# Optimization experiments

Measured on AMD Instinct MI355X. Metric: run time of the kernel, lower is better.

The kernel has to match this reference:

```python
import jax, jax.numpy as jnp
import numpy as np

NEG_BIG = -1e9

def setup_inputs() -> dict:
    key = jax.random.key(0)
    kq, kk, kv, kwq, kwk, kwv, km = jax.random.split(key, 7)
    B, S, d = 16, 1024, 512
    Q = jax.random.normal(kq, (B, S, d), dtype=jnp.float32)
    K = jax.random.normal(kk, (B, S, d), dtype=jnp.float32)
    V = jax.random.normal(kv, (B, S, d), dtype=jnp.float32)
    # nn.Linear weights [d, d]; torch applies x @ W.T
    WQ = jax.random.normal(kwq, (d, d), dtype=jnp.float32) / np.sqrt(d)
    WK = jax.random.normal(kwk, (d, d), dtype=jnp.float32) / np.sqrt(d)
    WV = jax.random.normal(kwv, (d, d), dtype=jnp.float32) / np.sqrt(d)
    mask = jax.random.randint(km, (B, S), 0, 2, dtype=jnp.int32)
    return {"Q": Q, "K": K, "V": V, "WQ": WQ, "WK": WK, "WV": WV, "mask": mask}


def reference(Q, K, V, WQ, WK, WV, mask):
    d = Q.shape[-1]
    q = jnp.einsum('bsd,ed->bse', Q, WQ)
    k = jnp.einsum('bsd,ed->bse', K, WK)
    v = jnp.einsum('bsd,ed->bse', V, WV)
    scores = jnp.einsum('bqd,bkd->bqk', q, k) / jnp.sqrt(jnp.float32(d))
    attn = jax.nn.softmax(scores, axis=-1)
    # Faithful to original: mask applied AFTER softmax with -1e9 fill
    m = mask[:, None, :]  # [B,1,S] broadcast over query dim
    attn = jnp.where(m == 0, jnp.float32(NEG_BIG), attn)
    out = jnp.einsum('bqk,bkd->bqd', attn, v)
    return (out, attn)
```

## Files before the change

### kernel.cpp

```cpp
#include <hip/hip_runtime.h>
#include <hip/hip_bf16.h>

typedef float f32x4 __attribute__((ext_vector_type(4)));
typedef __bf16 bf16x8 __attribute__((ext_vector_type(8)));
typedef unsigned short u16x8 __attribute__((ext_vector_type(8)));
typedef unsigned short u16x4 __attribute__((ext_vector_type(4)));
typedef int i32x4 __attribute__((ext_vector_type(4)));

#define NEG_BIG_F (-1000000000.0f)
#define SCALE_F 0.044194173824159216f

__device__ __forceinline__ unsigned short f2bf(float f) {
  unsigned int u = __float_as_uint(f);
  u += 0x7FFFu + ((u >> 16) & 1u);
  return (unsigned short)(u >> 16);
}

__device__ __forceinline__ float bf2f(unsigned short h) {
  return __uint_as_float((unsigned int)h << 16);
}

__device__ __forceinline__ u16x8 cvt8(f32x4 a, f32x4 b) {
  u16x8 r;
  r[0] = f2bf(a[0]); r[1] = f2bf(a[1]); r[2] = f2bf(a[2]); r[3] = f2bf(a[3]);
  r[4] = f2bf(b[0]); r[5] = f2bf(b[1]); r[6] = f2bf(b[2]); r[7] = f2bf(b[3]);
  return r;
}

__device__ __forceinline__ void gload16(const void* g, char* l) {
  __builtin_amdgcn_global_load_lds(
      (const __attribute__((address_space(1))) unsigned int*)g,
      (__attribute__((address_space(3))) unsigned int*)l, 16, 0, 0);
}

__global__ __launch_bounds__(256) void cvtWX(
    const float* __restrict__ w0, const float* __restrict__ w1,
    const float* __restrict__ w2, const float* __restrict__ Q,
    const float* __restrict__ Kx, const float* __restrict__ V,
    unsigned short* __restrict__ wb, unsigned short* __restrict__ xb)
{
  const int z = blockIdx.z;
  if (z == 0) {
    if (blockIdx.x >= 384) return;
    const int i = (blockIdx.x * 256 + threadIdx.x) * 8;
    const float* src = i < 262144 ? w0 : (i < 524288 ? w1 : w2);
    const int j = i & 262143;
    f32x4 a = *(const f32x4*)(src + j);
    f32x4 b = *(const f32x4*)(src + j + 4);
    *(u16x8*)&wb[i] = cvt8(a, b);
  } else {
    const float* src = z == 1 ? Q : (z == 2 ? Kx : V);
    unsigned short* dst = xb + (size_t)(z - 1) * 8388608;
    const int i = (blockIdx.x * 256 + threadIdx.x) * 8;
    f32x4 a = *(const f32x4*)(src + i);
    f32x4 b = *(const f32x4*)(src + i + 4);
    *(u16x8*)&dst[i] = cvt8(a, b);
  }
}

__global__ __launch_bounds__(512, 2) void proj_all(
    const unsigned short* __restrict__ xb, const unsigned short* __restrict__ wb,
    unsigned short* __restrict__ qb, unsigned short* __restrict__ kb,
    unsigned short* __restrict__ vt)
{
  __shared__ __align__(16) unsigned short As[2][256][32];
  __shared__ __align__(16) unsigned short Bs[2][256][32];

  const int bid = blockIdx.x;
  const int tid = threadIdx.x;
  const int lane = tid & 63, wave = tid >> 6;
  const int wr = (wave >> 2) * 128, wc = (wave & 3) * 64;
  const int fr = lane & 15, fq = lane >> 4;

  const unsigned short* Abase;
  const unsigned short* Bbase;
  int m0, n0;
  if (bid < 256) {
    const int z = bid >> 7, rem = bid & 127;
    m0 = (rem & 63) * 256; n0 = (rem >> 6) * 256;
    Abase = xb + (size_t)z * 8388608 + (size_t)m0 * 512;
    Bbase = wb + (size_t)z * 262144 + (size_t)n0 * 512;
  } else {
    const int c0 = bid - 256;
    const int b = c0 >> 3;
    m0 = ((c0 >> 2) & 1) * 256;
    n0 = (c0 & 3) * 256;
    Abase = wb + 524288 + (size_t)m0 * 512;
    Bbase = xb + 16777216 + ((size_t)b * 1024 + n0) * 512;
  }

  f32x4 acc[8][4] = {};

  const unsigned short* gA[2]; char* lA[2];
  const unsigned short* gB[2]; char* lB[2];
  #pragma unroll
  for (int i = 0; i < 2; i++) {
    const int c = tid + 512 * i, row = c >> 2, slot = c & 3;
    const int sw = (slot ^ ((row >> 1) & 3)) * 8;
    gA[i] = Abase + (size_t)row * 512 + sw;
    gB[i] = Bbase + (size_t)row * 512 + sw;
    lA[i] = (char*)&As[0][0][0] + c * 16;
    lB[i] = (char*)&Bs[0][0][0] + c * 16;
  }

  #pragma unroll
  for (int i = 0; i < 2; i++) { gload16(gA[i], lA[i]); gload16(gB[i], lB[i]); }

  int cur = 0;
  for (int kt = 0; kt < 512; kt += 32) {
    const int nb = cur ^ 1;
    if (kt < 480) {
      #pragma unroll
      for (int i = 0; i < 2; i++) {
        gload16(gA[i] + kt + 32, lA[i] + nb * 16384);
        gload16(gB[i] + kt + 32, lB[i] + nb * 16384);
      }
      asm volatile("s_waitcnt vmcnt(4) lgkmcnt(0)" ::: "memory");
    } else {
      asm volatile("s_waitcnt vmcnt(0) lgkmcnt(0)" ::: "memory");
    }
    __builtin_amdgcn_sched_barrier(0);
    __builtin_amdgcn_s_barrier();

    bf16x8 bv[4];
    #pragma unroll
    for (int nf = 0; nf < 4; nf++) {
      const int br = wc + nf * 16 + fr;
      bv[nf] = *(const bf16x8*)&Bs[cur][br][(fq ^ ((br >> 1) & 3)) * 8];
    }
    #pragma unroll
    for (int mf = 0; mf < 8; mf++) {
      const int ar = wr + mf * 16 + fr;
      bf16x8 av = *(const bf16x8*)&As[cur][ar][(fq ^ ((ar >> 1) & 3)) * 8];
      #pragma unroll
      for (int nf = 0; nf < 4; nf++)
        acc[mf][nf] = __builtin_amdgcn_mfma_f32_16x16x32_bf16(av, bv[nf], acc[mf][nf], 0, 0, 0);
    }
    __builtin_amdgcn_s_barrier();
    cur = nb;
  }

  if (bid < 256) {
    unsigned short* Y = (bid >> 7) ? kb : qb;
    #pragma unroll
    for (int mf = 0; mf < 8; mf++)
      #pragma unroll
      for (int nf = 0; nf < 4; nf++)
        #pragma unroll
        for (int rr = 0; rr < 4; rr++) {
          const int m = m0 + wr + mf * 16 + fq * 4 + rr;
          const int n = n0 + wc + nf * 16 + fr;
          Y[(size_t)m * 512 + n] = f2bf(acc[mf][nf][rr]);
        }
  } else {
    const int b = (bid - 256) >> 3;
    #pragma unroll
    for (int mf = 0; mf < 8; mf++)
      #pragma unroll
      for (int nf = 0; nf < 4; nf++)
        #pragma unroll
        for (int rr = 0; rr < 4; rr++) {
          const int e = m0 + wr + mf * 16 + fq * 4 + rr;
          const int s = n0 + wc + nf * 16 + fr;
          vt[((size_t)b * 512 + e) * 1024 + s] = f2bf(acc[mf][nf][rr]);
        }
  }
}

__global__ __launch_bounds__(512, 2) void score_mv(
    const unsigned short* __restrict__ qb, const unsigned short* __restrict__ kb,
    const unsigned short* __restrict__ vt, const int* __restrict__ mask,
    unsigned short* __restrict__ P, float* __restrict__ partial,
    float* __restrict__ mvsum)
{
  __shared__ __align__(16) unsigned short As[2][256][32];
  __shared__ __align__(16) unsigned short Bs[2][256][32];

  const int bid = blockIdx.x;
  const int tid = threadIdx.x;

  if (bid >= 256) {
    const int row = (bid - 256) * 8 + (tid >> 6);
    const int b = row >> 9;
    const int lane = tid & 63;
    const unsigned short* vr = vt + (size_t)row * 1024 + lane * 16;
    const int* mr = mask + b * 1024 + lane * 16;
    u16x8 v0 = *(const u16x8*)(vr);
    u16x8 v1 = *(const u16x8*)(vr + 8);
    float s = 0.f;
    #pragma unroll
    for (int j = 0; j < 8; j++) {
      if (!mr[j])     s += bf2f(v0[j]);
      if (!mr[8 + j]) s += bf2f(v1[j]);
    }
    #pragma unroll
    for (int o = 32; o > 0; o >>= 1) s += __shfl_xor(s, o);
    if (lane == 0) mvsum[row] = s;
    return;
  }

  const int xcd = bid & 7, idx = bid >> 3;
  const int bz = xcd * 2 + (idx >> 4);
  const int tile = idx & 15;
  const int m0 = (tile & 3) * 256, n0 = ((tile >> 2) & 3) * 256;
  const int lane = tid & 63, wave = tid >> 6;
  const int wr = (wave >> 2) * 128, wc = (wave & 3) * 64;
  const int fr = lane & 15, fq = lane >> 4;

  f32x4 acc[8][4] = {};

  const unsigned short* gA[2]; char* lA[2];
  const unsigned short* gB[2]; char* lB[2];
  #pragma unroll
  for (int i = 0; i < 2; i++) {
    const int c = tid + 512 * i, row = c >> 2, slot = c & 3;
    const int sw = (slot ^ ((row >> 1) & 3)) * 8;
    gA[i] = qb + ((size_t)bz * 1024 + m0 + row) * 512 + sw;
    gB[i] = kb + ((size_t)bz * 1024 + n0 + row) * 512 + sw;
    lA[i] = (char*)&As[0][0][0] + c * 16;
    lB[i] = (char*)&Bs[0][0][0] + c * 16;
  }

  #pragma unroll
  for (int i = 0; i < 2; i++) { gload16(gA[i], lA[i]); gload16(gB[i], lB[i]); }

  int cur = 0;
  for (int kt = 0; kt < 512; kt += 32) {
    const int nb = cur ^ 1;
    if (kt < 480) {
      #pragma unroll
      for (int i = 0; i < 2; i++) {
        gload16(gA[i] + kt + 32, lA[i] + nb * 16384);
        gload16(gB[i] + kt + 32, lB[i] + nb * 16384);
      }
      asm volatile("s_waitcnt vmcnt(4) lgkmcnt(0)" ::: "memory");
    } else {
      asm volatile("s_waitcnt vmcnt(0) lgkmcnt(0)" ::: "memory");
    }
    __builtin_amdgcn_sched_barrier(0);
    __builtin_amdgcn_s_barrier();

    bf16x8 bv[4];
    #pragma unroll
    for (int nf = 0; nf < 4; nf++) {
      const int br = wc + nf * 16 + fr;
      bv[nf] = *(const bf16x8*)&Bs[cur][br][(fq ^ ((br >> 1) & 3)) * 8];
    }
    #pragma unroll
    for (int mf = 0; mf < 8; mf++) {
      const int ar = wr + mf * 16 + fr;
      bf16x8 av = *(const bf16x8*)&As[cur][ar][(fq ^ ((ar >> 1) & 3)) * 8];
      #pragma unroll
      for (int nf = 0; nf < 4; nf++)
        acc[mf][nf] = __builtin_amdgcn_mfma_f32_16x16x32_bf16(av, bv[nf], acc[mf][nf], 0, 0, 0);
    }
    __builtin_amdgcn_s_barrier();
    cur = nb;
  }

  int mcol[4];
  #pragma unroll
  for (int nf = 0; nf < 4; nf++)
    mcol[nf] = mask[bz * 1024 + n0 + wc + nf * 16 + fr];

  unsigned short* Pb = P + ((size_t)bz << 20);
  const int slot = ((tile >> 2) & 3) * 4 + (wave & 3);
  #pragma unroll
  for (int mf = 0; mf < 8; mf++) {
    #pragma unroll
    for (int rr = 0; rr < 4; rr++) {
      const int m = m0 + wr + mf * 16 + fq * 4 + rr;
      float e = 0.f;
      #pragma unroll
      for (int nf = 0; nf < 4; nf++) {
        const float ev = __expf(acc[mf][nf][rr] * SCALE_F);
        e += ev;
        Pb[(size_t)m * 1024 + n0 + wc + nf * 16 + fr] =
            mcol[nf] ? f2bf(ev) : (unsigned short)0;
      }
      e += __shfl_xor(e, 1); e += __shfl_xor(e, 2);
      e += __shfl_xor(e, 4); e += __shfl_xor(e, 8);
      if (fr == 0)
        partial[(size_t)slot * 16384 + bz * 1024 + m] = e;
    }
  }
}

__global__ __launch_bounds__(512) void pv_attn(
    const unsigned short* __restrict__ P, const unsigned short* __restrict__ vt,
    const float* __restrict__ partial, const float* __restrict__ mvsum,
    const int* __restrict__ mask,
    float* __restrict__ out, float* __restrict__ attn)
{
  __shared__ __align__(16) unsigned short As[2][64][32];
  __shared__ __align__(16) unsigned short Bs[2][512][32];
  __shared__ float inv_l[64];

  const int tid = threadIdx.x;
  const int lin = blockIdx.x;
  const int xcd = lin & 7, idx = lin >> 3;
  const int bz = xcd * 2 + (idx >> 4);
  const int m0 = (idx & 15) * 64;
  const int lane = tid & 63, wave = tid >> 6;
  const int n0 = wave * 64;
  const int fr = lane & 15, fq = lane >> 4;

  f32x4 acc[4][4] = {};

  if (tid < 64) {
    float s = 0.f;
    #pragma unroll
    for (int p = 0; p < 16; p++) s += partial[(size_t)p * 16384 + bz * 1024 + m0 + tid];
    inv_l[tid] = 1.0f / s;
  }

  const unsigned short* gA = nullptr; char* lA = nullptr;
  if (tid < 256) {
    const int row = tid >> 2, slot = tid & 3;
    gA = P + ((size_t)bz << 20) + (size_t)(m0 + row) * 1024 + (slot ^ ((row >> 1) & 3)) * 8;
    lA = (char*)&As[0][0][0] + tid * 16;
  }
  const unsigned short* gB[4]; char* lB[4];
  #pragma unroll
  for (int i = 0; i < 4; i++) {
    const int c = tid + 512 * i, row = c >> 2, slot = c & 3;
    gB[i] = vt + ((size_t)bz * 512 + row) * 1024 + (slot ^ ((row >> 1) & 3)) * 8;
    lB[i] = (char*)&Bs[0][0][0] + c * 16;
  }

  const int arow = tid >> 3, acol = (tid & 7) * 4;
  const int aslot8 = ((acol >> 3) ^ ((arow >> 1) & 3)) * 8 + (acol & 7);
  float* arp = attn + ((size_t)bz * 1024 + m0 + arow) * 1024 + acol;
  const int* mrp = mask + bz * 1024 + acol;

  if (tid < 256) gload16(gA, lA);
  #pragma unroll
  for (int i = 0; i < 4; i++) gload16(gB[i], lB[i]);
  __syncthreads();

  int cur = 0;
  for (int t = 0; t < 32; t++) {
    const int nb = cur ^ 1;
    const int kt = t * 32;
    if (t < 31) {
      if (tid < 256) gload16(gA + kt + 32, lA + nb * 4096);
      #pragma unroll
      for (int i = 0; i < 4; i++) gload16(gB[i] + kt + 32, lB[i] + nb * 32768);
      if (wave < 4) asm volatile("s_waitcnt vmcnt(5) lgkmcnt(0)" ::: "memory");
      else          asm volatile("s_waitcnt vmcnt(4) lgkmcnt(0)" ::: "memory");
    } else {
      asm volatile("s_waitcnt vmcnt(0) lgkmcnt(0)" ::: "memory");
    }
    __builtin_amdgcn_sched_barrier(0);
    __builtin_amdgcn_s_barrier();

    bf16x8 af[4], bv[4];
    #pragma unroll
    for (int mf = 0; mf < 4; mf++) {
      const int ar = mf * 16 + fr;
      af[mf] = *(const bf16x8*)&As[cur][ar][(fq ^ ((ar >> 1) & 3)) * 8];
    }
    #pragma unroll
    for (int nf = 0; nf < 4; nf++) {
      const int br = n0 + nf * 16 + fr;
      bv[nf] = *(const bf16x8*)&Bs[cur][br][(fq ^ ((br >> 1) & 3)) * 8];
    }
    #pragma unroll
    for (int mf = 0; mf < 4; mf++)
      #pragma unroll
      for (int nf = 0; nf < 4; nf++)
        acc[mf][nf] = __builtin_amdgcn_mfma_f32_16x16x32_bf16(af[mf], bv[nf], acc[mf][nf], 0, 0, 0);

    {
      const u16x4 pv4 = *(const u16x4*)&As[cur][arow][aslot8];
      const i32x4 mv = *(const i32x4*)(mrp + kt);
      const float iv = inv_l[arow];
      f32x4 o;
      o[0] = mv[0] ? bf2f(pv4[0]) * iv : NEG_BIG_F;
      o[1] = mv[1] ? bf2f(pv4[1]) * iv : NEG_BIG_F;
      o[2] = mv[2] ? bf2f(pv4[2]) * iv : NEG_BIG_F;
      o[3] = mv[3] ? bf2f(pv4[3]) * iv : NEG_BIG_F;
      *(f32x4*)(arp + kt) = o;
    }
    __builtin_amdgcn_s_barrier();
    cur = nb;
  }

  float mvv[4];
  #pragma unroll
  for (int nf = 0; nf < 4; nf++)
    mvv[nf] = mvsum[bz * 512 + n0 + nf * 16 + fr];
  #pragma unroll
  for (int mf = 0; mf < 4; mf++)
    #pragma unroll
    for (int rr = 0; rr < 4; rr++) {
      const int m = m0 + mf * 16 + fq * 4 + rr;
      const float iv = inv_l[mf * 16 + fq * 4 + rr];
      #pragma unroll
      for (int nf = 0; nf < 4; nf++)
        out[((size_t)bz * 1024 + m) * 512 + n0 + nf * 16 + fr] =
            iv * acc[mf][nf][rr] + NEG_BIG_F * mvv[nf];
    }
}

extern "C" void kernel_launch(void* const* d_in, const int* in_sizes, int n_in,
                              void* d_out, int out_size, void* d_ws, size_t ws_size,
                              hipStream_t stream)
{
  const float* Q  = (const float*)d_in[0];
  const float* Kx = (const float*)d_in[1];
  const float* V  = (const float*)d_in[2];
  const float* WQ = (const float*)d_in[3];
  const float* WK = (const float*)d_in[4];
  const float* WV = (const float*)d_in[5];
  const int* mask = (const int*)d_in[6];

  const int B = 16, S = 1024, D = 512;
  float* out_f  = (float*)d_out;
  float* attn_f = out_f + (size_t)B * S * D;
  unsigned short* Pbuf = (unsigned short*)d_out;
  unsigned short* xb = (unsigned short*)attn_f;

  unsigned short* qb = (unsigned short*)d_ws;
  unsigned short* kb = qb + (size_t)B * S * D;
  unsigned short* vt = kb + (size_t)B * S * D;
  unsigned short* wb = vt + (size_t)B * S * D;
  float* partial = (float*)(wb + 786432);
  float* mvsum = partial + 262144;

  cvtWX<<<dim3(4096, 1, 4), 256, 0, stream>>>(WQ, WK, WV, Q, Kx, V, wb, xb);
  proj_all<<<dim3(384), 512, 0, stream>>>(xb, wb, qb, kb, vt);
  score_mv<<<dim3(1280), 512, 0, stream>>>(qb, kb, vt, mask, Pbuf, partial, mvsum);
  pv_attn<<<dim3(256), 512, 0, stream>>>(Pbuf, vt, partial, mvsum, mask, out_f, attn_f);
}
```

Measured before the change: 138.1 us.

## Fuse V fp32-to-bf16 conversion into the V projection GEMM

The separate conversion pass no longer converts V to bf16. The V-projection blocks in proj_all now stream fp32 V straight into LDS and convert to bf16 in registers before the MFMA. The V tiles shrink to 128x256 and the grid grows to 512 blocks, so LDS use rises to 80KB with fp32 B tiles. This removes one read and one write of V in bf16, at the cost of more LDS traffic and in-loop conversion work, and possibly lower occupancy.

```diff
diff --git a/kernel.cpp b/kernel.cpp
--- a/kernel.cpp
+++ b/kernel.cpp
@@ -27,6 +27,10 @@
   return r;
 }
 
+__device__ __forceinline__ bf16x8 u2b(u16x8 u) {
+  union { u16x8 u; bf16x8 b; } c; c.u = u; return c.b;
+}
+
 __device__ __forceinline__ void gload16(const void* g, char* l) {
   __builtin_amdgcn_global_load_lds(
       (const __attribute__((address_space(1))) unsigned int*)g,
@@ -36,7 +40,7 @@
 __global__ __launch_bounds__(256) void cvtWX(
     const float* __restrict__ w0, const float* __restrict__ w1,
     const float* __restrict__ w2, const float* __restrict__ Q,
-    const float* __restrict__ Kx, const float* __restrict__ V,
+    const float* __restrict__ Kx,
     unsigned short* __restrict__ wb, unsigned short* __restrict__ xb)
 {
   const int z = blockIdx.z;
@@ -49,7 +53,7 @@
     f32x4 b = *(const f32x4*)(src + j + 4);
     *(u16x8*)&wb[i] = cvt8(a, b);
   } else {
-    const float* src = z == 1 ? Q : (z == 2 ? Kx : V);
+    const float* src = z == 1 ? Q : Kx;
     unsigned short* dst = xb + (size_t)(z - 1) * 8388608;
     const int i = (blockIdx.x * 256 + threadIdx.x) * 8;
     f32x4 a = *(const f32x4*)(src + i);
@@ -59,89 +63,80 @@
 }
 
 __global__ __launch_bounds__(512, 2) void proj_all(
-    const unsigned short* __restrict__ xb, const unsigned short* __restrict__ wb,
+    const unsigned short* __restrict__ xb, const float* __restrict__ V,
+    const unsigned short* __restrict__ wb,
     unsigned short* __restrict__ qb, unsigned short* __restrict__ kb,
     unsigned short* __restrict__ vt)
 {
-  __shared__ __align__(16) unsigned short As[2][256][32];
-  __shared__ __align__(16) unsigned short Bs[2][256][32];
+  __shared__ __align__(16) char pool[81920];
 
   const int bid = blockIdx.x;
   const int tid = threadIdx.x;
   const int lane = tid & 63, wave = tid >> 6;
-  const int wr = (wave >> 2) * 128, wc = (wave & 3) * 64;
   const int fr = lane & 15, fq = lane >> 4;
 
-  const unsigned short* Abase;
-  const unsigned short* Bbase;
-  int m0, n0;
   if (bid < 256) {
+    unsigned short (*As)[256][32] = (unsigned short (*)[256][32])pool;
+    unsigned short (*Bs)[256][32] = (unsigned short (*)[256][32])(pool + 32768);
+
     const int z = bid >> 7, rem = bid & 127;
-    m0 = (rem & 63) * 256; n0 = (rem >> 6) * 256;
-    Abase = xb + (size_t)z * 8388608 + (size_t)m0 * 512;
-    Bbase = wb + (size_t)z * 262144 + (size_t)n0 * 512;
-  } else {
-    const int c0 = bid - 256;
-    const int b = c0 >> 3;
-    m0 = ((c0 >> 2) & 1) * 256;
-    n0 = (c0 & 3) * 256;
-    Abase = wb + 524288 + (size_t)m0 * 512;
-    Bbase = xb + 16777216 + ((size_t)b * 1024 + n0) * 512;
-  }
-
-  f32x4 acc[8][4] = {};
-
-  const unsigned short* gA[2]; char* lA[2];
-  const unsigned short* gB[2]; char* lB[2];
-  #pragma unroll
-  for (int i = 0; i < 2; i++) {
-    const int c = tid + 512 * i, row = c >> 2, slot = c & 3;
-    const int sw = (slot ^ ((row >> 1) & 3)) * 8;
-    gA[i] = Abase + (size_t)row * 512 + sw;
-    gB[i] = Bbase + (size_t)row * 512 + sw;
-    lA[i] = (char*)&As[0][0][0] + c * 16;
-    lB[i] = (char*)&Bs[0][0][0] + c * 16;
-  }
-
-  #pragma unroll
-  for (int i = 0; i < 2; i++) { gload16(gA[i], lA[i]); gload16(gB[i], lB[i]); }
-
-  int cur = 0;
-  for (int kt = 0; kt < 512; kt += 32) {
-    const int nb = cur ^ 1;
-    if (kt < 480) {
-      #pragma unroll
-      for (int i = 0; i < 2; i++) {
-        gload16(gA[i] + kt + 32, lA[i] + nb * 16384);
-        gload16(gB[i] + kt + 32, lB[i] + nb * 16384);
-      }
-      asm volatile("s_waitcnt vmcnt(4) lgkmcnt(0)" ::: "memory");
-    } else {
-      asm volatile("s_waitcnt vmcnt(0) lgkmcnt(0)" ::: "memory");
-    }
-    __builtin_amdgcn_sched_barrier(0);
-    __builtin_amdgcn_s_barrier();
-
-    bf16x8 bv[4];
-    #pragma unroll
-    for (int nf = 0; nf < 4; nf++) {
-      const int br = wc + nf * 16 + fr;
-      bv[nf] = *(const bf16x8*)&Bs[cur][br][(fq ^ ((br >> 1) & 3)) * 8];
-    }
-    #pragma unroll
-    for (int mf = 0; mf < 8; mf++) {
-      const int ar = wr + mf * 16 + fr;
-      bf16x8 av = *(const bf16x8*)&As[cur][ar][(fq ^ ((ar >> 1) & 3)) * 8];
-      #pragma unroll
-      for (int nf = 0; nf < 4; nf++)
-        acc[mf][nf] = __builtin_amdgcn_mfma_f32_16x16x32_bf16(av, bv[nf], acc[mf][nf], 0, 0, 0);
-    }
-    __builtin_amdgcn_s_barrier();
-    cur = nb;
-  }
-
-  if (bid < 256) {
-    unsigned short* Y = (bid >> 7) ? kb : qb;
+    const int m0 = (rem & 63) * 256, n0 = (rem >> 6) * 256;
+    const unsigned short* Abase = xb + (size_t)z * 8388608 + (size_t)m0 * 512;
+    const unsigned short* Bbase = wb + (size_t)z * 262144 + (size_t)n0 * 512;
+    const int wr = (wave >> 2) * 128, wc = (wave & 3) * 64;
+
+    f32x4 acc[8][4] = {};
+
+    const unsigned short* gA[2]; char* lA[2];
+    const unsigned short* gB[2]; char* lB[2];
+    #pragma unroll
+    for (int i = 0; i < 2; i++) {
+      const int c = tid + 512 * i, row = c >> 2, slot = c & 3;
+      const int sw = (slot ^ ((row >> 1) & 3)) * 8;
+      gA[i] = Abase + (size_t)row * 512 + sw;
+      gB[i] = Bbase + (size_t)row * 512 + sw;
+      lA[i] = pool + c * 16;
+      lB[i] = pool + 32768 + c * 16;
+    }
+
+    #pragma unroll
+    for (int i = 0; i < 2; i++) { gload16(gA[i], lA[i]); gload16(gB[i], lB[i]); }
+
+    int cur = 0;
+    for (int kt = 0; kt < 512; kt += 32) {
+      const int nb = cur ^ 1;
+      if (kt < 480) {
+        #pragma unroll
+        for (int i = 0; i < 2; i++) {
+          gload16(gA[i] + kt + 32, lA[i] + nb * 16384);
+          gload16(gB[i] + kt + 32, lB[i] + nb * 16384);
+        }
+        asm volatile("s_waitcnt vmcnt(4) lgkmcnt(0)" ::: "memory");
+      } else {
+        asm volatile("s_waitcnt vmcnt(0) lgkmcnt(0)" ::: "memory");
+      }
+      __builtin_amdgcn_sched_barrier(0);
+      __builtin_amdgcn_s_barrier();
+
+      bf16x8 bv[4];
+      #pragma unroll
+      for (int nf = 0; nf < 4; nf++) {
+        const int br = wc + nf * 16 + fr;
+        bv[nf] = *(const bf16x8*)&Bs[cur][br][(fq ^ ((br >> 1) & 3)) * 8];
+      }
+      #pragma unroll
+      for (int mf = 0; mf < 8; mf++) {
+        const int ar = wr + mf * 16 + fr;
+        bf16x8 av = *(const bf16x8*)&As[cur][ar][(fq ^ ((ar >> 1) & 3)) * 8];
+        #pragma unroll
+        for (int nf = 0; nf < 4; nf++)
+          acc[mf][nf] = __builtin_amdgcn_mfma_f32_16x16x32_bf16(av, bv[nf], acc[mf][nf], 0, 0, 0);
+      }
+      __builtin_amdgcn_s_barrier();
+      cur = nb;
+    }
+
+    unsigned short* Y = z ? kb : qb;
     #pragma unroll
     for (int mf = 0; mf < 8; mf++)
       #pragma unroll
@@ -153,9 +148,69 @@
           Y[(size_t)m * 512 + n] = f2bf(acc[mf][nf][rr]);
         }
   } else {
-    const int b = (bid - 256) >> 3;
-    #pragma unroll
-    for (int mf = 0; mf < 8; mf++)
+    unsigned short (*As)[128][32] = (unsigned short (*)[128][32])pool;
+    float          (*Bf)[256][32] = (float (*)[256][32])(pool + 16384);
+
+    const int bid2 = bid - 256;
+    const int m0 = (bid2 & 3) * 128, n0 = ((bid2 >> 2) & 3) * 256, b = bid2 >> 4;
+    const int wr = (wave >> 2) * 64, wc = (wave & 3) * 64;
+    const unsigned short* wv = wb + 524288;
+
+    f32x4 acc[4][4] = {};
+
+    const int arw = tid >> 2, asl = tid & 3;
+    const unsigned short* gA = wv + (size_t)(m0 + arw) * 512 + (asl ^ ((arw >> 1) & 3)) * 8;
+    char* lA = pool + tid * 16;
+    const float* gB[4]; char* lB[4];
+    #pragma unroll
+    for (int i = 0; i < 4; i++) {
+      const int c = tid + 512 * i, row = c >> 3, slot = c & 7;
+      gB[i] = V + ((size_t)b * 1024 + n0 + row) * 512 + (slot ^ (row & 7)) * 4;
+      lB[i] = pool + 16384 + c * 16;
+    }
+
+    gload16(gA, lA);
+    #pragma unroll
+    for (int i = 0; i < 4; i++) gload16(gB[i], lB[i]);
+
+    int cur = 0;
+    for (int kt = 0; kt < 512; kt += 32) {
+      const int nb = cur ^ 1;
+      if (kt < 480) {
+        gload16(gA + kt + 32, lA + nb * 8192);
+        #pragma unroll
+        for (int i = 0; i < 4; i++) gload16(gB[i] + kt + 32, lB[i] + nb * 32768);
+        asm volatile("s_waitcnt vmcnt(5) lgkmcnt(0)" ::: "memory");
+      } else {
+        asm volatile("s_waitcnt vmcnt(0) lgkmcnt(0)" ::: "memory");
+      }
+      __builtin_amdgcn_sched_barrier(0);
+      __builtin_amdgcn_s_barrier();
+
+      bf16x8 av[4], bv[4];
+      #pragma unroll
+      for (int mf = 0; mf < 4; mf++) {
+        const int ar = wr + mf * 16 + fr;
+        av[mf] = *(const bf16x8*)&As[cur][ar][(fq ^ ((ar >> 1) & 3)) * 8];
+      }
+      #pragma unroll
+      for (int nf = 0; nf < 4; nf++) {
+        const int br = wc + nf * 16 + fr;
+        f32x4 lo = *(const f32x4*)&Bf[cur][br][((fq * 2)     ^ (br & 7)) * 4];
+        f32x4 hi = *(const f32x4*)&Bf[cur][br][((fq * 2 + 1) ^ (br & 7)) * 4];
+        bv[nf] = u2b(cvt8(lo, hi));
+      }
+      #pragma unroll
+      for (int mf = 0; mf < 4; mf++)
+        #pragma unroll
+        for (int nf = 0; nf < 4; nf++)
+          acc[mf][nf] = __builtin_amdgcn_mfma_f32_16x16x32_bf16(av[mf], bv[nf], acc[mf][nf], 0, 0, 0);
+      __builtin_amdgcn_s_barrier();
+      cur = nb;
+    }
+
+    #pragma unroll
+    for (int mf = 0; mf < 4; mf++)
       #pragma unroll
       for (int nf = 0; nf < 4; nf++)
         #pragma unroll
@@ -428,8 +483,8 @@
   float* partial = (float*)(wb + 786432);
   float* mvsum = partial + 262144;
 
-  cvtWX<<<dim3(4096, 1, 4), 256, 0, stream>>>(WQ, WK, WV, Q, Kx, V, wb, xb);
-  proj_all<<<dim3(384), 512, 0, stream>>>(xb, wb, qb, kb, vt);
+  cvtWX<<<dim3(4096, 1, 3), 256, 0, stream>>>(WQ, WK, WV, Q, Kx, wb, xb);
+  proj_all<<<dim3(512), 512, 0, stream>>>(xb, V, wb, qb, kb, vt);
   score_mv<<<dim3(1280), 512, 0, stream>>>(qb, kb, vt, mask, Pbuf, partial, mvsum);
   pv_attn<<<dim3(256), 512, 0, stream>>>(Pbuf, vt, partial, mvsum, mask, out_f, attn_f);
 }
```

Result: no change. 137.2 us (-0.7%).
